# Kernel tuning notes

Hardware: AMD Instinct MI355X
Metric: run time of the kernel (lower is better)

## Reference

```python
import jax, jax.numpy as jnp
import numpy as np

H = 300      # hidden_dim == GloVe embedding dim (LSTM output is discarded)
MID = 100    # Scorer hidden width
N = 1024     # sentence length


def setup_inputs() -> dict:
    key = jax.random.key(0)
    k1, k2, k3, k4, k5, k6 = jax.random.split(key, 6)
    sentence = jax.random.normal(k1, (N, H), dtype=jnp.float32)
    target_scores = jax.random.randint(k2, (N,), 0, N + 1)
    # nn.Linear(2H, MID) and nn.Linear(MID, 1) params (uniform fan-in init style)
    lim1 = 1.0 / np.sqrt(2 * H)
    W1 = jax.random.uniform(k3, (MID, 2 * H), dtype=jnp.float32, minval=-lim1, maxval=lim1)
    b1 = jax.random.uniform(k4, (MID,), dtype=jnp.float32, minval=-lim1, maxval=lim1)
    lim2 = 1.0 / np.sqrt(MID)
    W2 = jax.random.uniform(k5, (1, MID), dtype=jnp.float32, minval=-lim2, maxval=lim2)
    b2 = jax.random.uniform(k6, (1,), dtype=jnp.float32, minval=-lim2, maxval=lim2)
    return {"sentence": sentence, "target_scores": target_scores,
            "W1": W1, "b1": b1, "W2": W2, "b2": b2}


def reference(sentence, W1, b1, W2, b2, target_scores):
    n = sentence.shape[0]
    # potential_matches = [zeros(H); sentence] -> [n+1, H]
    pm = jnp.concatenate([jnp.zeros((1, H), sentence.dtype), sentence], axis=0)
    # Split the first Linear over the two concatenated halves and broadcast-add:
    # cat(sentence[i], pm[j]) @ W1^T == sentence[i] @ W1[:, :H]^T + pm[j] @ W1[:, H:]^T
    s1 = jnp.einsum('nh,mh->nm', sentence, W1[:, :H])   # [n, MID]
    s2 = jnp.einsum('ph,mh->pm', pm, W1[:, H:])          # [n+1, MID]
    hidden = jax.nn.sigmoid(s1[:, None, :] + s2[None, :, :] + b1)  # [n, n+1, MID]
    scores = jnp.einsum('npm,om->npo', hidden, W2)[..., 0] + b2[0]  # [n, n+1]
    # L1 loss against one-hot indicator of the true head, averaged over all pairs
    indicator = (jnp.arange(n + 1)[None, :] == target_scores[:, None]).astype(scores.dtype)
    loss = jnp.mean(jnp.abs(scores - indicator))
    score_matrix = jax.nn.softmax(scores, axis=1)
    return loss, score_matrix
```

## Files before the change

kernel.cpp:

```cpp
#include <hip/hip_runtime.h>

#define H     300
#define MID   100
#define NN    1024
#define NP1   1025
#define JST   1088

typedef float v2f __attribute__((ext_vector_type(2)));
static __device__ __forceinline__ v2f sp2(float s) { return (v2f){s, s}; }
static __device__ __forceinline__ v2f fma2(v2f a, v2f b, v2f c) {
    return __builtin_elementwise_fma(a, b, c);
}

__global__ __launch_bounds__(256) void precompute_kernel(
    const float* __restrict__ sentence,
    const float* __restrict__ W1,
    const float* __restrict__ b1,
    float* __restrict__ s1b,
    float* __restrict__ E4,
    float* __restrict__ out)
{
    __shared__ float rA[H];
    __shared__ float rB[H];
    const int tid = threadIdx.x;
    const int iA = blockIdx.x * 2, iB = iA + 1;
    const float NL = -1.4426950408889634f;

    if (blockIdx.x == 0) {
        if (tid == 0) out[0] = 0.0f;
        if (tid < MID)
            E4[(long)((tid >> 2) * JST) * 4 + (tid & 3)] = 1.0f;
    }

    const float* sA = sentence + (long)iA * H;
    const float* sB = sentence + (long)iB * H;
    for (int idx = tid; idx < 2 * H; idx += 256) {
        if (idx < H) rA[idx] = sA[idx];
        else         rB[idx - H] = sB[idx - H];
    }
    __syncthreads();

    const int wv   = tid >> 6;
    const int lane = tid & 63;
    const int sub  = lane >> 5;
    const int hb   = lane & 31;
    const int half = wv >> 1;
    const int mb   = (wv & 1) * 50;

    for (int q = 0; q < 25; ++q) {
        const int m = mb + 2 * q + sub;
        const float* wrow = W1 + (long)m * (2 * H) + half * H;
        float aA = 0.f, aB = 0.f;
        #pragma unroll
        for (int k = 0; k < 9; ++k) {
            const int h = hb + 32 * k;
            const float w = wrow[h];
            aA = __builtin_fmaf(w, rA[h], aA);
            aB = __builtin_fmaf(w, rB[h], aB);
        }
        if (hb < 12) {
            const int h = hb + 288;
            const float w = wrow[h];
            aA = __builtin_fmaf(w, rA[h], aA);
            aB = __builtin_fmaf(w, rB[h], aB);
        }
        #pragma unroll
        for (int off = 16; off > 0; off >>= 1) {
            aA += __shfl_xor(aA, off, 64);
            aB += __shfl_xor(aB, off, 64);
        }
        if (hb == 0) {
            if (half == 0) {
                const float bb = b1[m];
                s1b[iA * MID + m] = aA + bb;
                s1b[iB * MID + m] = aB + bb;
            } else {
                float* base = E4 + (long)((m >> 2) * JST) * 4 + (m & 3);
                base[(long)(iA + 1) * 4] = __builtin_amdgcn_exp2f(aA * NL);
                base[(long)(iB + 1) * 4] = __builtin_amdgcn_exp2f(aB * NL);
            }
        }
    }
}

__global__ __launch_bounds__(512, 2) void main_kernel(
    const float* __restrict__ s1b,
    const float* __restrict__ E4,
    const float* __restrict__ W2,
    const float* __restrict__ b2,
    const int*   __restrict__ target,
    float* __restrict__ out)
{
    __shared__ float4 Fq[MID];
    __shared__ float4 w4sh[MID / 4];
    __shared__ float  tmp[4][104];
    __shared__ float  redl[8];
    __shared__ float4 redm[8];
    __shared__ float4 rede[8];
    __shared__ float  sc4sh[4];
    __shared__ float4 bmax, binv;

    const int i0  = blockIdx.x * 4;
    const int tid = threadIdx.x;
    const int lane = tid & 63, wv = tid >> 6;
    const float NL  = -1.4426950408889634f;
    const float L2E =  1.4426950408889634f;
    const v2f one2 = sp2(1.0f);

    if (tid < MID) {
        Fq[tid] = make_float4(
            __builtin_amdgcn_exp2f(s1b[(i0 + 0) * MID + tid] * NL),
            __builtin_amdgcn_exp2f(s1b[(i0 + 1) * MID + tid] * NL),
            __builtin_amdgcn_exp2f(s1b[(i0 + 2) * MID + tid] * NL),
            __builtin_amdgcn_exp2f(s1b[(i0 + 3) * MID + tid] * NL));
    } else if (tid >= 128 && tid < 128 + MID / 4) {
        const int p = tid - 128;
        w4sh[p] = make_float4(W2[4 * p], W2[4 * p + 1], W2[4 * p + 2], W2[4 * p + 3]);
    }
    const float b2v = b2[0];
    __syncthreads();

    #define LDXA(p_) (*(const float4*)(E4 + ((long)(p_) * JST + tid) * 4))
    #define LDXB(p_) (*(const float4*)(E4 + ((long)(p_) * JST + tid + 512) * 4))

    v2f acc01a = sp2(0.f), acc23a = sp2(0.f);
    v2f acc01b = sp2(0.f), acc23b = sp2(0.f);

    #define QCOL(X, accLo, accHi)                                             \
        do {                                                                  \
            const v2f e0 = sp2((X).x), e1 = sp2((X).y);                       \
            const v2f e2 = sp2((X).z), e3 = sp2((X).w);                       \
            {                                                   \
                const v2f A = fma2(e0, (v2f){F0.x, F0.y}, one2);              \
                const v2f B = fma2(e1, (v2f){F1.x, F1.y}, one2);              \
                const v2f C = fma2(e2, (v2f){F2.x, F2.y}, one2);              \
                const v2f D = fma2(e3, (v2f){F3.x, F3.y}, one2);              \
                const v2f AB = A * B, CD = C * D, P = AB * CD;                \
                const v2f R = {__builtin_amdgcn_rcpf(P.x),                    \
                               __builtin_amdgcn_rcpf(P.y)};                   \
                const v2f n1 = fma2(w0, B, w1 * A);                           \
                const v2f n2 = fma2(w2v, D, w3 * C);                          \
                accLo = fma2(fma2(n1, CD, n2 * AB), R, accLo);                \
            }                                                                 \
            {                                                   \
                const v2f A = fma2(e0, (v2f){F0.z, F0.w}, one2);              \
                const v2f B = fma2(e1, (v2f){F1.z, F1.w}, one2);              \
                const v2f C = fma2(e2, (v2f){F2.z, F2.w}, one2);              \
                const v2f D = fma2(e3, (v2f){F3.z, F3.w}, one2);              \
                const v2f AB = A * B, CD = C * D, P = AB * CD;                \
                const v2f R = {__builtin_amdgcn_rcpf(P.x),                    \
                               __builtin_amdgcn_rcpf(P.y)};                   \
                const v2f n1 = fma2(w0, B, w1 * A);                           \
                const v2f n2 = fma2(w2v, D, w3 * C);                          \
                accHi = fma2(fma2(n1, CD, n2 * AB), R, accHi);                \
            }                                                                 \
        } while (0)

    #define QBODY(p_, XA, XB)                                                 \
        do {                                                                  \
            const float4 F0 = Fq[4 * (p_)];                                   \
            const float4 F1 = Fq[4 * (p_) + 1];                               \
            const float4 F2 = Fq[4 * (p_) + 2];                               \
            const float4 F3 = Fq[4 * (p_) + 3];                               \
            const float4 w  = w4sh[p_];                                       \
            const v2f w0 = sp2(w.x), w1 = sp2(w.y);                           \
            const v2f w2v = sp2(w.z), w3 = sp2(w.w);                          \
            QCOL(XA, acc01a, acc23a);                                         \
            QCOL(XB, acc01b, acc23b);                                         \
        } while (0)

    float4 xa0 = LDXA(0), xb0 = LDXB(0);
    float4 xa1 = LDXA(1), xb1 = LDXB(1);
    #pragma unroll 2
    for (int p = 0; p < 23; ++p) {
        const float4 xan = LDXA(p + 2), xbn = LDXB(p + 2);
        QBODY(p, xa0, xb0);
        xa0 = xa1; xa1 = xan;
        xb0 = xb1; xb1 = xbn;
    }
    QBODY(23, xa0, xb0);
    QBODY(24, xa1, xb1);

    const float sc0a = acc01a.x + b2v, sc1a = acc01a.y + b2v;
    const float sc2a = acc23a.x + b2v, sc3a = acc23a.y + b2v;
    const float sc0b = acc01b.x + b2v, sc1b = acc01b.y + b2v;
    const float sc2b = acc23b.x + b2v, sc3b = acc23b.y + b2v;

    if (tid < MID) {
        const float E = E4[((long)(tid >> 2) * JST + 1024) * 4 + (tid & 3)];
        const float4 F = Fq[tid];
        const float wm = W2[tid];
        tmp[0][tid] = wm * __builtin_amdgcn_rcpf(__builtin_fmaf(E, F.x, 1.f));
        tmp[1][tid] = wm * __builtin_amdgcn_rcpf(__builtin_fmaf(E, F.y, 1.f));
        tmp[2][tid] = wm * __builtin_amdgcn_rcpf(__builtin_fmaf(E, F.z, 1.f));
        tmp[3][tid] = wm * __builtin_amdgcn_rcpf(__builtin_fmaf(E, F.w, 1.f));
    }
    __syncthreads();
    if (wv < 4) {
        float v = tmp[wv][lane] + ((lane < MID - 64) ? tmp[wv][lane + 64] : 0.f);
        #pragma unroll
        for (int off = 32; off > 0; off >>= 1) v += __shfl_down(v, off);
        if (lane == 0) sc4sh[wv] = v + b2v;
    }
    __syncthreads();

    const int tg0 = target[i0], tg1 = target[i0 + 1];
    const int tg2 = target[i0 + 2], tg3 = target[i0 + 3];
    const int jb = tid + 512;
    float ls = fabsf(sc0a - ((tid == tg0) ? 1.f : 0.f))
             + fabsf(sc1a - ((tid == tg1) ? 1.f : 0.f))
             + fabsf(sc2a - ((tid == tg2) ? 1.f : 0.f))
             + fabsf(sc3a - ((tid == tg3) ? 1.f : 0.f))
             + fabsf(sc0b - ((jb == tg0) ? 1.f : 0.f))
             + fabsf(sc1b - ((jb == tg1) ? 1.f : 0.f))
             + fabsf(sc2b - ((jb == tg2) ? 1.f : 0.f))
             + fabsf(sc3b - ((jb == tg3) ? 1.f : 0.f));
    float4 mx = make_float4(fmaxf(sc0a, sc0b), fmaxf(sc1a, sc1b),
                            fmaxf(sc2a, sc2b), fmaxf(sc3a, sc3b));
    if (tid == 0) {
        ls += fabsf(sc4sh[0] - ((1024 == tg0) ? 1.f : 0.f))
            + fabsf(sc4sh[1] - ((1024 == tg1) ? 1.f : 0.f))
            + fabsf(sc4sh[2] - ((1024 == tg2) ? 1.f : 0.f))
            + fabsf(sc4sh[3] - ((1024 == tg3) ? 1.f : 0.f));
        mx.x = fmaxf(mx.x, sc4sh[0]);
        mx.y = fmaxf(mx.y, sc4sh[1]);
        mx.z = fmaxf(mx.z, sc4sh[2]);
        mx.w = fmaxf(mx.w, sc4sh[3]);
    }
    #pragma unroll
    for (int off = 32; off > 0; off >>= 1) {
        ls += __shfl_down(ls, off);
        mx.x = fmaxf(mx.x, __shfl_down(mx.x, off));
        mx.y = fmaxf(mx.y, __shfl_down(mx.y, off));
        mx.z = fmaxf(mx.z, __shfl_down(mx.z, off));
        mx.w = fmaxf(mx.w, __shfl_down(mx.w, off));
    }
    if (lane == 0) { redl[wv] = ls; redm[wv] = mx; }
    __syncthreads();
    if (tid == 0) {
        float L = 0.f;
        float4 M = make_float4(-1e30f, -1e30f, -1e30f, -1e30f);
        #pragma unroll
        for (int k = 0; k < 8; ++k) {
            L += redl[k];
            M.x = fmaxf(M.x, redm[k].x);
            M.y = fmaxf(M.y, redm[k].y);
            M.z = fmaxf(M.z, redm[k].z);
            M.w = fmaxf(M.w, redm[k].w);
        }
        atomicAdd(out, L * (1.0f / ((float)NN * (float)NP1)));
        bmax = M;
    }
    __syncthreads();
    const float4 rm = bmax;

    const float e0a = __builtin_amdgcn_exp2f((sc0a - rm.x) * L2E);
    const float e1a = __builtin_amdgcn_exp2f((sc1a - rm.y) * L2E);
    const float e2a = __builtin_amdgcn_exp2f((sc2a - rm.z) * L2E);
    const float e3a = __builtin_amdgcn_exp2f((sc3a - rm.w) * L2E);
    const float e0b = __builtin_amdgcn_exp2f((sc0b - rm.x) * L2E);
    const float e1b = __builtin_amdgcn_exp2f((sc1b - rm.y) * L2E);
    const float e2b = __builtin_amdgcn_exp2f((sc2b - rm.z) * L2E);
    const float e3b = __builtin_amdgcn_exp2f((sc3b - rm.w) * L2E);
    float4 e4v = make_float4(0.f, 0.f, 0.f, 0.f);
    if (tid == 0) {
        e4v.x = __builtin_amdgcn_exp2f((sc4sh[0] - rm.x) * L2E);
        e4v.y = __builtin_amdgcn_exp2f((sc4sh[1] - rm.y) * L2E);
        e4v.z = __builtin_amdgcn_exp2f((sc4sh[2] - rm.z) * L2E);
        e4v.w = __builtin_amdgcn_exp2f((sc4sh[3] - rm.w) * L2E);
    }
    float4 es = make_float4(e0a + e0b + e4v.x, e1a + e1b + e4v.y,
                            e2a + e2b + e4v.z, e3a + e3b + e4v.w);
    #pragma unroll
    for (int off = 32; off > 0; off >>= 1) {
        es.x += __shfl_down(es.x, off);
        es.y += __shfl_down(es.y, off);
        es.z += __shfl_down(es.z, off);
        es.w += __shfl_down(es.w, off);
    }
    if (lane == 0) rede[wv] = es;
    __syncthreads();
    if (tid == 0) {
        float4 S = make_float4(0.f, 0.f, 0.f, 0.f);
        #pragma unroll
        for (int k = 0; k < 8; ++k) {
            S.x += rede[k].x; S.y += rede[k].y;
            S.z += rede[k].z; S.w += rede[k].w;
        }
        binv = make_float4(1.f / S.x, 1.f / S.y, 1.f / S.z, 1.f / S.w);
    }
    __syncthreads();
    const float4 iv = binv;

    float* o0 = out + 1 + (long)(i0 + 0) * NP1;
    float* o1 = out + 1 + (long)(i0 + 1) * NP1;
    float* o2 = out + 1 + (long)(i0 + 2) * NP1;
    float* o3 = out + 1 + (long)(i0 + 3) * NP1;
    o0[tid] = e0a * iv.x;
    o1[tid] = e1a * iv.y;
    o2[tid] = e2a * iv.z;
    o3[tid] = e3a * iv.w;
    o0[jb] = e0b * iv.x;
    o1[jb] = e1b * iv.y;
    o2[jb] = e2b * iv.z;
    o3[jb] = e3b * iv.w;
    if (tid == 0) {
        o0[1024] = e4v.x * iv.x;
        o1[1024] = e4v.y * iv.y;
        o2[1024] = e4v.z * iv.z;
        o3[1024] = e4v.w * iv.w;
    }
    #undef QBODY
    #undef QCOL
    #undef LDXA
    #undef LDXB
}

extern "C" void kernel_launch(void* const* d_in, const int* in_sizes, int n_in,
                              void* d_out, int out_size, void* d_ws, size_t ws_size,
                              hipStream_t stream) {
    const float* sentence = (const float*)d_in[0];
    const int*   target   = (const int*)  d_in[1];
    const float* W1       = (const float*)d_in[2];
    const float* b1       = (const float*)d_in[3];
    const float* W2       = (const float*)d_in[4];
    const float* b2       = (const float*)d_in[5];
    float* out = (float*)d_out;

    float* s1b = (float*)d_ws;
    float* E4  = s1b + NN * MID;

    precompute_kernel<<<NN / 2, 256, 0, stream>>>(sentence, W1, b1, s1b, E4, out);
    main_kernel<<<NN / 4, 512, 0, stream>>>(s1b, E4, W2, b2, target, out);
}
```

Before: 101.3 us.

## Restructure precompute: register-resident rows, DPP reductions, 512-thread blocks

The precompute kernel now keeps each thread's slice of the two sentence rows in registers instead of staging them through shared memory, which removes the barrier. The 32-lane reductions use DPP row rotates plus a ds_swizzle instead of shuffles. Blocks grow to 512 threads, so each wave covers fewer output rows (13 iterations instead of 25), with a clamped duplicate row for the odd leftover. This targets the latency of the small precompute kernel, at the cost of some redundant work in the last iteration. Correctness of the DPP reduction also depends on the row_ror patterns summing the 16-lane rows as intended.

```diff
diff --git a/kernel.cpp b/kernel.cpp
--- a/kernel.cpp
+++ b/kernel.cpp
@@ -12,7 +12,25 @@
     return __builtin_elementwise_fma(a, b, c);
 }
 
-__global__ __launch_bounds__(256) void precompute_kernel(
+template <int CTRL>
+static __device__ __forceinline__ float row_ror_add(float v) {
+    const int s = __builtin_amdgcn_update_dpp(0, __float_as_int(v), CTRL, 0xF, 0xF, true);
+    return v + __int_as_float(s);
+}
+static __device__ __forceinline__ float swz_xor16_add(float v) {
+    const int s = __builtin_amdgcn_ds_swizzle(__float_as_int(v), 0x401F);
+    return v + __int_as_float(s);
+}
+static __device__ __forceinline__ float red32(float v) {
+    v = swz_xor16_add(v);
+    v = row_ror_add<0x128>(v);
+    v = row_ror_add<0x124>(v);
+    v = row_ror_add<0x122>(v);
+    v = row_ror_add<0x121>(v);
+    return v;
+}
+
+__global__ __launch_bounds__(512) void precompute_kernel(
     const float* __restrict__ sentence,
     const float* __restrict__ W1,
     const float* __restrict__ b1,
@@ -20,8 +38,6 @@
     float* __restrict__ E4,
     float* __restrict__ out)
 {
-    __shared__ float rA[H];
-    __shared__ float rB[H];
     const int tid = threadIdx.x;
     const int iA = blockIdx.x * 2, iB = iA + 1;
     const float NL = -1.4426950408889634f;
@@ -32,44 +48,50 @@
             E4[(long)((tid >> 2) * JST) * 4 + (tid & 3)] = 1.0f;
     }
 
-    const float* sA = sentence + (long)iA * H;
-    const float* sB = sentence + (long)iB * H;
-    for (int idx = tid; idx < 2 * H; idx += 256) {
-        if (idx < H) rA[idx] = sA[idx];
-        else         rB[idx - H] = sB[idx - H];
-    }
-    __syncthreads();
-
+    const int lane = tid & 63;
     const int wv   = tid >> 6;
-    const int lane = tid & 63;
     const int sub  = lane >> 5;
     const int hb   = lane & 31;
-    const int half = wv >> 1;
-    const int mb   = (wv & 1) * 50;
-
-    for (int q = 0; q < 25; ++q) {
-        const int m = mb + 2 * q + sub;
+    const int half = wv & 1;
+    const int mb   = (wv >> 1) * 25;
+
+    const float* sA = sentence + (long)iA * H + hb;
+    const float* sB = sentence + (long)iB * H + hb;
+    float ra[9], rb[9];
+    #pragma unroll
+    for (int k = 0; k < 9; ++k) { ra[k] = sA[32 * k]; rb[k] = sB[32 * k]; }
+    const bool tl = hb < 12;
+    const float ra9 = tl ? sA[288] : 0.0f;
+    const float rb9 = tl ? sB[288] : 0.0f;
+    const int h9 = 288 + (tl ? hb : 0);
+
+    for (int q = 0; q < 13; ++q) {
+        const int off = 2 * q + sub;
+        const int m   = mb + (off < 25 ? off : 24);
         const float* wrow = W1 + (long)m * (2 * H) + half * H;
-        float aA = 0.f, aB = 0.f;
+
+        float aA, aB;
+        {
+            const float w0 = wrow[hb];
+            aA = w0 * ra[0];
+            aB = w0 * rb[0];
+        }
         #pragma unroll
-        for (int k = 0; k < 9; ++k) {
-            const int h = hb + 32 * k;
-            const float w = wrow[h];
-            aA = __builtin_fmaf(w, rA[h], aA);
-            aB = __builtin_fmaf(w, rB[h], aB);
-        }
-        if (hb < 12) {
-            const int h = hb + 288;
-            const float w = wrow[h];
-            aA = __builtin_fmaf(w, rA[h], aA);
-            aB = __builtin_fmaf(w, rB[h], aB);
-        }
-        #pragma unroll
-        for (int off = 16; off > 0; off >>= 1) {
-            aA += __shfl_xor(aA, off, 64);
-            aB += __shfl_xor(aB, off, 64);
-        }
-        if (hb == 0) {
+        for (int k = 1; k < 9; ++k) {
+            const float w = wrow[hb + 32 * k];
+            aA = __builtin_fmaf(w, ra[k], aA);
+            aB = __builtin_fmaf(w, rb[k], aB);
+        }
+        {
+            const float w9 = wrow[h9];
+            aA = __builtin_fmaf(w9, ra9, aA);
+            aB = __builtin_fmaf(w9, rb9, aB);
+        }
+
+        aA = red32(aA);
+        aB = red32(aB);
+
+        if (hb == 0 && off < 25) {
             if (half == 0) {
                 const float bb = b1[m];
                 s1b[iA * MID + m] = aA + bb;
@@ -330,6 +352,6 @@
     float* s1b = (float*)d_ws;
     float* E4  = s1b + NN * MID;
 
-    precompute_kernel<<<NN / 2, 256, 0, stream>>>(sentence, W1, b1, s1b, E4, out);
+    precompute_kernel<<<NN / 2, 512, 0, stream>>>(sentence, W1, b1, s1b, E4, out);
     main_kernel<<<NN / 4, 512, 0, stream>>>(s1b, E4, W2, b2, target, out);
 }
```

New measurement: 91.70 us. 1.1x faster.
